# Kernel optimization log

Measured on AMD Instinct MI355X. Metric: run time of the kernel, lower is better.

## Reference

```python
import jax, jax.numpy as jnp
import numpy as np

DIM = 128
N_GNN = 3
B, N1, N2 = 8, 128, 512
VDW_N = 6.0
DEV_VDW = 0.2
MAX_VDW, MIN_VDW = 0.0356, 0.0178
DM_MIN = 0.5


def setup_inputs() -> dict:
    key = jax.random.key(0)
    ks = jax.random.split(key, 24)
    f32 = jnp.float32
    h1 = jax.random.normal(ks[0], (B, N1, 54), f32)
    h2 = jax.random.normal(ks[1], (B, N2, 54), f32)
    a1 = (jax.random.uniform(ks[2], (B, N1, N1)) < 0.1).astype(f32)
    adj1 = jnp.clip(a1 + jnp.swapaxes(a1, 1, 2) + jnp.eye(N1, dtype=f32), 0.0, 1.0)
    a2 = (jax.random.uniform(ks[3], (B, N2, N2)) < 0.05).astype(f32)
    adj2 = jnp.clip(a2 + jnp.swapaxes(a2, 1, 2) + jnp.eye(N2, dtype=f32), 0.0, 1.0)
    A_int = (jax.random.uniform(ks[4], (B, 8, N1, N2)) < 0.05).astype(f32)
    pos1 = jax.random.uniform(ks[5], (B, N1, 3), f32) * 30.0
    pos2 = jax.random.uniform(ks[6], (B, N2, 3), f32) * 30.0
    rotor = jax.random.uniform(ks[7], (B,), f32) * 10.0
    vdw_radius1 = 1.0 + jax.random.uniform(ks[8], (B, N1), f32)
    vdw_radius2 = 1.0 + jax.random.uniform(ks[9], (B, N2), f32)
    delta_uff = jax.random.uniform(ks[10], (B,), f32)
    no_metal1 = jnp.ones((B, N1), f32)
    no_metal2 = jnp.ones((B, N2), f32)
    s = 0.1
    node_W = jax.random.normal(ks[11], (54, DIM), f32) * s
    gat_W = jax.random.normal(ks[12], (N_GNN, DIM, DIM), f32) * s
    gat_b = jnp.zeros((N_GNN, DIM), f32)
    gat_A = jax.random.normal(ks[13], (N_GNN, DIM, DIM), f32) * s
    gate_W = jax.random.normal(ks[14], (N_GNN, 2 * DIM), f32) * s
    gate_b = jnp.zeros((N_GNN,), f32)
    vdwA_W1 = jax.random.normal(ks[15], (2 * DIM, 128), f32) * s
    vdwA_b1 = jnp.zeros((128,), f32)
    vdwA_W2 = jax.random.normal(ks[16], (128,), f32) * s
    vdwA_b2 = jnp.zeros((1,), f32)
    vdwB_W1 = jax.random.normal(ks[17], (2 * DIM, 128), f32) * s
    vdwB_b1 = jnp.zeros((128,), f32)
    vdwB_W2 = jax.random.normal(ks[18], (128,), f32) * s
    vdwB_b2 = jnp.zeros((1,), f32)
    hbond_coeff = jnp.array([1.0], f32)
    hydrophobic_coeff = jnp.array([0.5], f32)
    vdw_coeff = jnp.array([1.0], f32)
    rotor_coeff = jnp.array([0.5], f32)
    return dict(h1=h1, adj1=adj1, h2=h2, adj2=adj2, A_int=A_int, pos1=pos1, pos2=pos2,
                rotor=rotor, vdw_radius1=vdw_radius1, vdw_radius2=vdw_radius2,
                delta_uff=delta_uff, no_metal1=no_metal1, no_metal2=no_metal2,
                node_W=node_W, gat_W=gat_W, gat_b=gat_b, gat_A=gat_A, gate_W=gate_W,
                gate_b=gate_b, vdwA_W1=vdwA_W1, vdwA_b1=vdwA_b1, vdwA_W2=vdwA_W2,
                vdwA_b2=vdwA_b2, vdwB_W1=vdwB_W1, vdwB_b1=vdwB_b1, vdwB_W2=vdwB_W2,
                vdwB_b2=vdwB_b2, hbond_coeff=hbond_coeff,
                hydrophobic_coeff=hydrophobic_coeff, vdw_coeff=vdw_coeff,
                rotor_coeff=rotor_coeff)


def _gat(x, adj, W, b, A, gW, gb):
    # PIGNet GAT_gate: attention softmax over axis=1, masked by adj, gated residual.
    h = x @ W + b                                   # [B,N,D]
    e = jnp.einsum('bil,bkl->bik', h @ A, h)        # [B,N,N]
    e = e + jnp.swapaxes(e, 1, 2)
    att = jnp.where(adj > 0, e, -9e15)
    att = jax.nn.softmax(att, axis=1) * adj
    h_prime = jax.nn.relu(jnp.einsum('bij,bjk->bik', att, h))
    coeff = jax.nn.sigmoid(jnp.concatenate([x, h_prime], -1) @ gW + gb)[..., None]
    return coeff * x + (1.0 - coeff) * h_prime


def _pair_mlp(g1, g2, W1, b1, w2, b2):
    # Equivalent to Linear(cat[h1_rep,h2_rep]) without materializing the 2D concat.
    z = (jnp.einsum('bik,kh->bih', g1, W1[:DIM])[:, :, None, :]
         + jnp.einsum('bjk,kh->bjh', g2, W1[DIM:])[:, None, :, :] + b1)  # [B,N1,N2,128]
    return jax.nn.relu(z) @ w2 + b2                 # [B,N1,N2]


def _forward(h1, adj1, h2, adj2, A_int, pos1, pos2, rotor, vdw_radius1, vdw_radius2,
             delta_uff, no_metal1, no_metal2, node_W, gat_W, gat_b, gat_A, gate_W,
             gate_b, vdwA_W1, vdwA_b1, vdwA_W2, vdwA_b2, vdwB_W1, vdwB_b1, vdwB_W2,
             vdwB_b2, hbond_coeff, hydrophobic_coeff, vdw_coeff, rotor_coeff):
    g1 = h1 @ node_W
    g2 = h2 @ node_W
    for i in range(N_GNN):
        g1 = _gat(g1, adj1, gat_W[i], gat_b[i], gat_A[i], gate_W[i], gate_b[i])
        g2 = _gat(g2, adj2, gat_W[i], gat_b[i], gat_A[i], gate_W[i], gate_b[i])
    diff = pos1[:, :, None, :] - pos2[:, None, :, :]
    dm = jnp.sqrt(jnp.sum(diff * diff, -1) + 1e-10)   # [B,N1,N2]
    dm = jnp.where(dm < DM_MIN, 1e10, dm)
    A_w = jax.nn.sigmoid(_pair_mlp(g1, g2, vdwA_W1, vdwA_b1, vdwA_W2, vdwA_b2))
    B_w = jnp.tanh(_pair_mlp(g1, g2, vdwB_W1, vdwB_b1, vdwB_W2, vdwB_b2)) * DEV_VDW
    dm0 = vdw_radius1[:, :, None] + vdw_radius2[:, None, :] + B_w
    # vdW 12-6 term
    dm0_safe = jnp.where(dm0 < 1e-4, 1.0, dm0)
    rN = (dm0_safe / dm) ** VDW_N
    evdw = jnp.minimum(rN * rN - 2.0 * rN, 100.0)
    mask12 = no_metal1[:, :, None] * no_metal2[:, None, :]
    Aamp = A_w * (MAX_VDW - MIN_VDW) + MIN_VDW
    E_vdw = jnp.sum(Aamp * evdw * mask12, axis=(1, 2))
    # hbond / hydrophobic terms use unfixed dm0
    dmd = dm - dm0
    hb = -(hbond_coeff * hbond_coeff)[0]
    hy = -(hydrophobic_coeff * hydrophobic_coeff)[0]
    E_hb1 = jnp.sum(jnp.clip(dmd * A_int[:, 1] / -0.7, 0.0, 1.0), axis=(1, 2)) * hb
    E_hb2 = jnp.sum(jnp.clip(dmd * A_int[:, -1] / -0.7, 0.0, 1.0), axis=(1, 2)) * hb
    E_hp = jnp.sum(jnp.clip((-dmd + 1.5) * A_int[:, -2], 0.0, 1.0), axis=(1, 2)) * hy
    E_t = delta_uff * (vdw_coeff * vdw_coeff)[0]
    ret = jnp.stack([E_vdw, E_hb1, E_hb2, E_hp, E_t], -1)   # [B,5]
    ret = ret / (1.0 + (rotor_coeff * rotor_coeff)[0] * rotor[:, None])
    return ret


def reference(h1, adj1, h2, adj2, A_int, pos1, pos2, rotor, vdw_radius1, vdw_radius2,
              delta_uff, no_metal1, no_metal2, node_W, gat_W, gat_b, gat_A, gate_W,
              gate_b, vdwA_W1, vdwA_b1, vdwA_W2, vdwA_b2, vdwB_W1, vdwB_b1, vdwB_W2,
              vdwB_b2, hbond_coeff, hydrophobic_coeff, vdw_coeff, rotor_coeff):
    return _forward(h1, adj1, h2, adj2, A_int, pos1, pos2, rotor, vdw_radius1,
                    vdw_radius2, delta_uff, no_metal1, no_metal2, node_W, gat_W,
                    gat_b, gat_A, gate_W, gate_b, vdwA_W1, vdwA_b1, vdwA_W2,
                    vdwA_b2, vdwB_W1, vdwB_b1, vdwB_W2, vdwB_b2, hbond_coeff,
                    hydrophobic_coeff, vdw_coeff, rotor_coeff)
```

## Files before the change

### kernel.cpp

```cpp
#include <hip/hip_runtime.h>
#include <hip/hip_fp16.h>
#include <math.h>

#define D 128
#define NB 8
#define NN1 128
#define NN2 512
#define ROWS1 (NB * NN1)
#define ROWS2 (NB * NN2)
#define ROWS (ROWS1 + ROWS2)
#define CAP1 96
#define CAP2 160
#define CSR_ELEMS ((size_t)ROWS1 * CAP1 + (size_t)ROWS2 * CAP2)

typedef __half HT;

__device__ __forceinline__ void resolve_row(int row, int& base_row, size_t& cbase,
                                            int& N) {
    if (row < ROWS1) {
        base_row = row & ~127;
        cbase = (size_t)row * CAP1;
        N = NN1;
    } else {
        int r = row - ROWS1;
        base_row = ROWS1 + (r & ~511);
        cbase = (size_t)ROWS1 * CAP1 + (size_t)r * CAP2;
        N = NN2;
    }
}

__device__ __forceinline__ int swiz_row(int bid) {
    int batch = bid & 7, idx = bid >> 3;
    return (idx < NN1) ? batch * NN1 + idx
                       : ROWS1 + batch * NN2 + (idx - NN1);
}
__device__ __forceinline__ int swiz_row16(int bid) {
    int batch = bid & 7, gi = bid >> 3;
    return (gi < 8) ? batch * NN1 + gi * 16
                    : ROWS1 + batch * NN2 + (gi - 8) * 16;
}

__device__ __forceinline__ void load8h(const HT* p, float* o) {
    float4 raw = *(const float4*)p;
    const __half2* h2 = (const __half2*)&raw;
    float2 f0 = __half22float2(h2[0]);
    float2 f1 = __half22float2(h2[1]);
    float2 f2 = __half22float2(h2[2]);
    float2 f3 = __half22float2(h2[3]);
    o[0] = f0.x; o[1] = f0.y; o[2] = f1.x; o[3] = f1.y;
    o[4] = f2.x; o[5] = f2.y; o[6] = f3.x; o[7] = f3.y;
}

__global__ __launch_bounds__(128) void k_csrembed(
    const float* __restrict__ h1, const float* __restrict__ h2,
    const float* __restrict__ adj1, const float* __restrict__ adj2,
    const float* __restrict__ W, float* __restrict__ g,
    unsigned short* __restrict__ csr, int* __restrict__ nnz,
    float* __restrict__ out) {
    int row = swiz_row(blockIdx.x);
    int t = threadIdx.x;
    if (blockIdx.x == 0 && t < NB * 5) out[t] = 0.f;
    const float* src = (row < ROWS1) ? h1 + (size_t)row * 54
                                     : h2 + (size_t)(row - ROWS1) * 54;
    __shared__ float xr[56];
    if (t < 54) xr[t] = src[t];
    __syncthreads();
    float a0 = 0.f, a1 = 0.f;
#pragma unroll
    for (int k = 0; k < 54; k += 2) {
        a0 += xr[k] * W[k * D + t];
        if (k + 1 < 54) a1 += xr[k + 1] * W[(k + 1) * D + t];
    }
    g[(size_t)row * D + t] = a0 + a1;

    if (t < 64) {
        int base_row, N;
        size_t cbase;
        resolve_row(row, base_row, cbase, N);
        int cap = (row < ROWS1) ? CAP1 : CAP2;
        const float* arow = (row < ROWS1) ? adj1 + (size_t)row * NN1
                                          : adj2 + (size_t)(row - ROWS1) * NN2;
        int cnt = 0;
        for (int c0 = 0; c0 < N; c0 += 64) {
            float v = arow[c0 + t];
            unsigned long long m = __ballot(v > 0.f);
            int rank = __popcll(m & ((1ull << t) - 1ull));
            if (v > 0.f && cnt + rank < cap)
                csr[cbase + cnt + rank] = (unsigned short)(c0 + t);
            cnt += __popcll(m);
        }
        if (t == 0) nnz[row] = cnt < cap ? cnt : cap;
    }
}

__global__ __launch_bounds__(256) void k_h(const float* __restrict__ g,
                                           const float* __restrict__ W,
                                           const float* __restrict__ bias,
                                           const float* __restrict__ A,
                                           HT* __restrict__ h, HT* __restrict__ hA) {
    int row0 = swiz_row16(blockIdx.x);
    int t = threadIdx.x;
    int d = t & 127, rh = t >> 7;
    __shared__ float xs[16][D];
    __shared__ float hs[16][D];
    {
        int r = t >> 4, c = (t & 15) * 8;
        *(float4*)&xs[r][c] = *(const float4*)&g[((size_t)row0 + r) * D + c];
        *(float4*)&xs[r][c + 4] = *(const float4*)&g[((size_t)row0 + r) * D + c + 4];
    }
    __syncthreads();
    float bv = bias[d];
    float acc[8];
#pragma unroll
    for (int u = 0; u < 8; ++u) acc[u] = bv;
    for (int k0 = 0; k0 < D; k0 += 4) {
        float w0 = W[(k0 + 0) * D + d];
        float w1 = W[(k0 + 1) * D + d];
        float w2 = W[(k0 + 2) * D + d];
        float w3 = W[(k0 + 3) * D + d];
#pragma unroll
        for (int u = 0; u < 8; ++u) {
            float4 xv = *(const float4*)&xs[rh * 8 + u][k0];
            acc[u] += xv.x * w0 + xv.y * w1 + xv.z * w2 + xv.w * w3;
        }
    }
#pragma unroll
    for (int u = 0; u < 8; ++u) {
        int r = rh * 8 + u;
        h[((size_t)row0 + r) * D + d] = __float2half(acc[u]);
        hs[r][d] = acc[u];
    }
    __syncthreads();
    float acc2[8];
#pragma unroll
    for (int u = 0; u < 8; ++u) acc2[u] = 0.f;
    for (int k0 = 0; k0 < D; k0 += 4) {
        float w0 = A[(k0 + 0) * D + d];
        float w1 = A[(k0 + 1) * D + d];
        float w2 = A[(k0 + 2) * D + d];
        float w3 = A[(k0 + 3) * D + d];
#pragma unroll
        for (int u = 0; u < 8; ++u) {
            float4 xv = *(const float4*)&hs[rh * 8 + u][k0];
            acc2[u] += xv.x * w0 + xv.y * w1 + xv.z * w2 + xv.w * w3;
        }
    }
#pragma unroll
    for (int u = 0; u < 8; ++u)
        hA[((size_t)row0 + rh * 8 + u) * D + d] = __float2half(acc2[u]);
}

__global__ __launch_bounds__(128) void k_Ssp(const HT* __restrict__ h,
                                             const HT* __restrict__ hA,
                                             const unsigned short* __restrict__ csr,
                                             const int* __restrict__ nnz,
                                             float* __restrict__ svals,
                                             float2* __restrict__ rowstat) {
    int row = swiz_row(blockIdx.x);
    int t = threadIdx.x;
    int base_row, N;
    size_t cbase;
    resolve_row(row, base_row, cbase, N);
    int n = nnz[row];
    int grp = t >> 4, u = t & 15;
    float hi[8], ai[8];
    load8h(h + (size_t)row * D + u * 8, hi);
    load8h(hA + (size_t)row * D + u * 8, ai);
    __shared__ float sv[CAP2];
    for (int s0 = 0; s0 < n; s0 += 16) {
        int sa = s0 + grp;
        int sb = sa + 8;
        float pa = 0.f, pb = 0.f;
        if (sa < n) {
            int jrow = base_row + csr[cbase + sa];
            float hj[8], aj[8];
            load8h(h + (size_t)jrow * D + u * 8, hj);
            load8h(hA + (size_t)jrow * D + u * 8, aj);
#pragma unroll
            for (int q = 0; q < 8; ++q) pa += hi[q] * aj[q] + ai[q] * hj[q];
        }
        if (sb < n) {
            int jrow = base_row + csr[cbase + sb];
            float hj[8], aj[8];
            load8h(h + (size_t)jrow * D + u * 8, hj);
            load8h(hA + (size_t)jrow * D + u * 8, aj);
#pragma unroll
            for (int q = 0; q < 8; ++q) pb += hi[q] * aj[q] + ai[q] * hj[q];
        }
#pragma unroll
        for (int o = 8; o > 0; o >>= 1) {
            pa += __shfl_xor(pa, o);
            pb += __shfl_xor(pb, o);
        }
        if (u == 0) {
            if (sa < n) sv[sa] = pa;
            if (sb < n) sv[sb] = pb;
        }
    }
    __syncthreads();
    if (t < 64) {
        float m = -3.4e38f;
        for (int s = t; s < n; s += 64) m = fmaxf(m, sv[s]);
#pragma unroll
        for (int o = 32; o > 0; o >>= 1) m = fmaxf(m, __shfl_xor(m, o));
        float sum = 0.f;
        for (int s = t; s < n; s += 64) sum += expf(sv[s] - m);
#pragma unroll
        for (int o = 32; o > 0; o >>= 1) sum += __shfl_xor(sum, o);
        if (t == 0) rowstat[row] = make_float2(m, 1.f / sum);
    }
    for (int s = t; s < n; s += 128) svals[cbase + s] = sv[s];
}

__global__ __launch_bounds__(128) void k_hpgate(const HT* __restrict__ hbuf,
                                                float* __restrict__ g,
                                                const float* __restrict__ svals,
                                                const float2* __restrict__ rowstat,
                                                const unsigned short* __restrict__ csr,
                                                const int* __restrict__ nnz,
                                                const float* __restrict__ gW,
                                                const float* __restrict__ gb) {
    int row = swiz_row(blockIdx.x);
    int d = threadIdx.x;
    int base_row, N;
    size_t cbase;
    resolve_row(row, base_row, cbase, N);
    int n = nnz[row];
    __shared__ float avals[CAP2];
    __shared__ int aidx[CAP2];
    __shared__ float red[128];
    for (int s = d; s < n; s += 128) {
        int jrow = base_row + csr[cbase + s];
        float2 st = rowstat[jrow];
        avals[s] = expf(svals[cbase + s] - st.x) * st.y;
        aidx[s] = jrow;
    }
    __syncthreads();
    float a[8];
#pragma unroll
    for (int u = 0; u < 8; ++u) a[u] = 0.f;
    int s = 0;
    for (; s + 8 <= n; s += 8) {
#pragma unroll
        for (int u = 0; u < 8; ++u)
            a[u] += avals[s + u] * __half2float(hbuf[(size_t)aidx[s + u] * D + d]);
    }
    for (; s < n; ++s)
        a[0] += avals[s] * __half2float(hbuf[(size_t)aidx[s] * D + d]);
    float hv = fmaxf(((a[0] + a[1]) + (a[2] + a[3])) + ((a[4] + a[5]) + (a[6] + a[7])),
                     0.f);
    float xv = g[(size_t)row * D + d];
    red[d] = xv * gW[d] + hv * gW[D + d];
    __syncthreads();
    for (int o = 64; o > 0; o >>= 1) {
        if (d < o) red[d] += red[d + o];
        __syncthreads();
    }
    float c = 1.f / (1.f + expf(-(red[0] + gb[0])));
    g[(size_t)row * D + d] = c * xv + (1.f - c) * hv;
}

__global__ __launch_bounds__(256) void k_pairpre(const float* __restrict__ g,
                                                 const float* __restrict__ WA,
                                                 const float* __restrict__ WB,
                                                 const float* __restrict__ bA,
                                                 const float* __restrict__ bB,
                                                 float* __restrict__ aA,
                                                 float* __restrict__ aB) {
    int row0 = swiz_row16(blockIdx.x);
    int t = threadIdx.x;
    int d = t & 127, rh = t >> 7;
    int g2 = (row0 >= ROWS1);
    const float* WAp = g2 ? WA + D * D : WA;
    const float* WBp = g2 ? WB + D * D : WB;
    __shared__ float xs[16][D];
    {
        int r = t >> 4, c = (t & 15) * 8;
        *(float4*)&xs[r][c] = *(const float4*)&g[((size_t)row0 + r) * D + c];
        *(float4*)&xs[r][c + 4] = *(const float4*)&g[((size_t)row0 + r) * D + c + 4];
    }
    __syncthreads();
    float bvA = g2 ? 0.f : bA[d];
    float bvB = g2 ? 0.f : bB[d];
    float accA[8], accB[8];
#pragma unroll
    for (int u = 0; u < 8; ++u) { accA[u] = bvA; accB[u] = bvB; }
    for (int k0 = 0; k0 < D; k0 += 4) {
        float wa0 = WAp[(k0 + 0) * D + d], wa1 = WAp[(k0 + 1) * D + d];
        float wa2 = WAp[(k0 + 2) * D + d], wa3 = WAp[(k0 + 3) * D + d];
        float wb0 = WBp[(k0 + 0) * D + d], wb1 = WBp[(k0 + 1) * D + d];
        float wb2 = WBp[(k0 + 2) * D + d], wb3 = WBp[(k0 + 3) * D + d];
#pragma unroll
        for (int u = 0; u < 8; ++u) {
            float4 xv = *(const float4*)&xs[rh * 8 + u][k0];
            accA[u] += xv.x * wa0 + xv.y * wa1 + xv.z * wa2 + xv.w * wa3;
            accB[u] += xv.x * wb0 + xv.y * wb1 + xv.z * wb2 + xv.w * wb3;
        }
    }
#pragma unroll
    for (int u = 0; u < 8; ++u) {
        int r = rh * 8 + u;
        aA[((size_t)row0 + r) * D + d] = accA[u];
        aB[((size_t)row0 + r) * D + d] = accB[u];
    }
}

__global__ __launch_bounds__(256) void k_pairz(
    const float* __restrict__ aA, const float* __restrict__ aB,
    const float* __restrict__ w2A, const float* __restrict__ w2B,
    const float* __restrict__ b2A, const float* __restrict__ b2B,
    const float* __restrict__ pos1, const float* __restrict__ pos2,
    const float* __restrict__ vr1, const float* __restrict__ vr2,
    const float* __restrict__ nm1, const float* __restrict__ nm2,
    const float* __restrict__ A_int, const float* __restrict__ rotor,
    const float* __restrict__ duff, const float* __restrict__ hbond,
    const float* __restrict__ hydro, const float* __restrict__ vdwc,
    const float* __restrict__ rotc, float* __restrict__ out) {
    int b = blockIdx.x & 7;
    int tile = blockIdx.x >> 3;
    int itile = tile >> 4, jtile = tile & 15;
    int i0 = itile * 32, j0 = jtile * 32;
    int t = threadIdx.x;
    int tx = t & 15, ty = t >> 4;
    __shared__ float A1a[32][20], A1b[32][20], A2a[32][20], A2b[32][20];
    __shared__ float w2As[128], w2Bs[128];
    __shared__ float zAs[32][33], zBs[32][33];
    __shared__ float redc[8][4];
    if (t < 128) { w2As[t] = w2A[t]; w2Bs[t] = w2B[t]; }
    float zA[2][2] = {{0.f, 0.f}, {0.f, 0.f}};
    float zB[2][2] = {{0.f, 0.f}, {0.f, 0.f}};
    int half = t >> 7, idx = t & 127;
    int sr = idx >> 2, sc = (idx & 3) * 4;
    size_t grow = half ? (size_t)(ROWS1 + b * NN2 + j0 + sr)
                       : (size_t)(b * NN1 + i0 + sr);
    for (int hc = 0; hc < D; hc += 16) {
        __syncthreads();
        float4 va = *(const float4*)&aA[grow * D + hc + sc];
        float4 vb = *(const float4*)&aB[grow * D + hc + sc];
        if (half) { *(float4*)&A2a[sr][sc] = va; *(float4*)&A2b[sr][sc] = vb; }
        else      { *(float4*)&A1a[sr][sc] = va; *(float4*)&A1b[sr][sc] = vb; }
        __syncthreads();
#pragma unroll
        for (int hh = 0; hh < 16; hh += 4) {
            float4 wA = *(const float4*)&w2As[hc + hh];
            float4 wB = *(const float4*)&w2Bs[hc + hh];
            float4 xA0 = *(const float4*)&A1a[ty][hh];
            float4 xA1 = *(const float4*)&A1a[ty + 16][hh];
            float4 xB0 = *(const float4*)&A1b[ty][hh];
            float4 xB1 = *(const float4*)&A1b[ty + 16][hh];
            float4 yA0 = *(const float4*)&A2a[tx][hh];
            float4 yA1 = *(const float4*)&A2a[tx + 16][hh];
            float4 yB0 = *(const float4*)&A2b[tx][hh];
            float4 yB1 = *(const float4*)&A2b[tx + 16][hh];
#define RD4(xx, yy, ww) (fmaxf(xx.x + yy.x, 0.f) * ww.x + fmaxf(xx.y + yy.y, 0.f) * ww.y + \
                         fmaxf(xx.z + yy.z, 0.f) * ww.z + fmaxf(xx.w + yy.w, 0.f) * ww.w)
            zA[0][0] += RD4(xA0, yA0, wA); zA[0][1] += RD4(xA0, yA1, wA);
            zA[1][0] += RD4(xA1, yA0, wA); zA[1][1] += RD4(xA1, yA1, wA);
            zB[0][0] += RD4(xB0, yB0, wB); zB[0][1] += RD4(xB0, yB1, wB);
            zB[1][0] += RD4(xB1, yB0, wB); zB[1][1] += RD4(xB1, yB1, wB);
#undef RD4
        }
    }
#pragma unroll
    for (int u = 0; u < 2; ++u)
#pragma unroll
        for (int v = 0; v < 2; ++v) {
            zAs[ty + 16 * u][tx + 16 * v] = zA[u][v];
            zBs[ty + 16 * u][tx + 16 * v] = zB[u][v];
        }
    __syncthreads();
    int j2 = t & 31, ig = t >> 5;
    int jg = j0 + j2;
    size_t j_off = (size_t)b * NN2 + jg;
    float p2x = pos2[j_off * 3 + 0], p2y = pos2[j_off * 3 + 1], p2z = pos2[j_off * 3 + 2];
    float r2 = vr2[j_off], m2 = nm2[j_off];
    float zb2A = b2A[0], zb2B = b2B[0];
    float eV[4], e1[4], e2[4], eH[4];
#pragma unroll
    for (int ii = 0; ii < 4; ++ii) {
        int il = ig * 4 + ii;
        int iglob = i0 + il;
        size_t i_off = (size_t)b * NN1 + iglob;
        float zAv = zAs[il][j2] + zb2A;
        float zBv = zBs[il][j2] + zb2B;
        float dx = pos1[i_off * 3 + 0] - p2x;
        float dy = pos1[i_off * 3 + 1] - p2y;
        float dz = pos1[i_off * 3 + 2] - p2z;
        float dm = sqrtf(dx * dx + dy * dy + dz * dz + 1e-10f);
        if (dm < 0.5f) dm = 1e10f;
        float A_w = 1.f / (1.f + expf(-zAv));
        float B_w = tanhf(zBv) * 0.2f;
        float dm0 = vr1[i_off] + r2 + B_w;
        float dm0s = (dm0 < 1e-4f) ? 1.f : dm0;
        float rr = dm0s / dm;
        float rr2 = rr * rr;
        float rN = rr2 * rr2 * rr2;
        float evdw = fminf(rN * rN - 2.f * rN, 100.f);
        float mask = nm1[i_off] * m2;
        float Aamp = A_w * (0.0356f - 0.0178f) + 0.0178f;
        eV[ii] = Aamp * evdw * mask;
        float dmd = dm - dm0;
        size_t abase = (((size_t)b * 8) * NN1 + iglob) * NN2 + jg;
        float Ai1 = A_int[abase + (size_t)1 * NN1 * NN2];
        float Ai6 = A_int[abase + (size_t)6 * NN1 * NN2];
        float Ai7 = A_int[abase + (size_t)7 * NN1 * NN2];
        e1[ii] = fminf(fmaxf(dmd * Ai1 * (-1.f / 0.7f), 0.f), 1.f);
        e2[ii] = fminf(fmaxf(dmd * Ai7 * (-1.f / 0.7f), 0.f), 1.f);
        eH[ii] = fminf(fmaxf((1.5f - dmd) * Ai6, 0.f), 1.f);
    }
    float sV = (eV[0] + eV[1]) + (eV[2] + eV[3]);
    float s1 = (e1[0] + e1[1]) + (e1[2] + e1[3]);
    float s2 = (e2[0] + e2[1]) + (e2[2] + e2[3]);
    float sH = (eH[0] + eH[1]) + (eH[2] + eH[3]);
#pragma unroll
    for (int o = 16; o > 0; o >>= 1) {
        sV += __shfl_xor(sV, o);
        s1 += __shfl_xor(s1, o);
        s2 += __shfl_xor(s2, o);
        sH += __shfl_xor(sH, o);
    }
    if (j2 == 0) {
        redc[ig][0] = sV; redc[ig][1] = s1; redc[ig][2] = s2; redc[ig][3] = sH;
    }
    __syncthreads();
    if (t < 4) {
        float v = 0.f;
#pragma unroll
        for (int gg = 0; gg < 8; ++gg) v += redc[gg][t];
        float scl = 1.f / (1.f + rotc[0] * rotc[0] * rotor[b]);
        float coef;
        if (t == 0) coef = scl;
        else if (t == 3) coef = -hydro[0] * hydro[0] * scl;
        else coef = -hbond[0] * hbond[0] * scl;
        atomicAdd(&out[b * 5 + t], v * coef);
    }
    if (t == 4 && tile == 0) {
        float scl = 1.f / (1.f + rotc[0] * rotc[0] * rotor[b]);
        atomicAdd(&out[b * 5 + 4], duff[b] * vdwc[0] * vdwc[0] * scl);
    }
}

extern "C" void kernel_launch(void* const* d_in, const int* in_sizes, int n_in,
                              void* d_out, int out_size, void* d_ws, size_t ws_size,
                              hipStream_t stream) {
    const float* h1    = (const float*)d_in[0];
    const float* adj1  = (const float*)d_in[1];
    const float* h2    = (const float*)d_in[2];
    const float* adj2  = (const float*)d_in[3];
    const float* A_int = (const float*)d_in[4];
    const float* pos1  = (const float*)d_in[5];
    const float* pos2  = (const float*)d_in[6];
    const float* rotor = (const float*)d_in[7];
    const float* vr1   = (const float*)d_in[8];
    const float* vr2   = (const float*)d_in[9];
    const float* duff  = (const float*)d_in[10];
    const float* nm1   = (const float*)d_in[11];
    const float* nm2   = (const float*)d_in[12];
    const float* nodeW = (const float*)d_in[13];
    const float* gatW  = (const float*)d_in[14];
    const float* gatb  = (const float*)d_in[15];
    const float* gatA  = (const float*)d_in[16];
    const float* gateW = (const float*)d_in[17];
    const float* gateb = (const float*)d_in[18];
    const float* vA_W1 = (const float*)d_in[19];
    const float* vA_b1 = (const float*)d_in[20];
    const float* vA_W2 = (const float*)d_in[21];
    const float* vA_b2 = (const float*)d_in[22];
    const float* vB_W1 = (const float*)d_in[23];
    const float* vB_b1 = (const float*)d_in[24];
    const float* vB_W2 = (const float*)d_in[25];
    const float* vB_b2 = (const float*)d_in[26];
    const float* hbond = (const float*)d_in[27];
    const float* hydro = (const float*)d_in[28];
    const float* vdwc  = (const float*)d_in[29];
    const float* rotc  = (const float*)d_in[30];

    float* p = (float*)d_ws;
    float* g     = p; p += (size_t)ROWS * D;
    float* aA    = p; p += (size_t)ROWS * D;
    float* aB    = p; p += (size_t)ROWS * D;
    float* svals = p; p += CSR_ELEMS;
    float2* rowstat = (float2*)p; p += 2 * (size_t)ROWS;
    HT* hbuf  = (HT*)p; p += (size_t)ROWS * D / 2;
    HT* hAbuf = (HT*)p; p += (size_t)ROWS * D / 2;
    unsigned short* csr = (unsigned short*)p;
    int* nnz = (int*)(csr + CSR_ELEMS);
    float* outp = (float*)d_out;

    k_csrembed<<<ROWS, 128, 0, stream>>>(h1, h2, adj1, adj2, nodeW, g, csr, nnz, outp);

    for (int l = 0; l < 3; ++l) {
        const float* W  = gatW  + (size_t)l * D * D;
        const float* bb = gatb  + (size_t)l * D;
        const float* A  = gatA  + (size_t)l * D * D;
        const float* gW = gateW + (size_t)l * 2 * D;
        const float* gb = gateb + l;
        k_h<<<ROWS / 16, 256, 0, stream>>>(g, W, bb, A, hbuf, hAbuf);
        k_Ssp<<<ROWS, 128, 0, stream>>>(hbuf, hAbuf, csr, nnz, svals, rowstat);
        k_hpgate<<<ROWS, 128, 0, stream>>>(hbuf, g, svals, rowstat, csr, nnz, gW, gb);
    }

    k_pairpre<<<ROWS / 16, 256, 0, stream>>>(g, vA_W1, vB_W1, vA_b1, vB_b1, aA, aB);
    k_pairz<<<512, 256, 0, stream>>>(aA, aB, vA_W2, vB_W2, vA_b2, vB_b2,
                                     pos1, pos2, vr1, vr2, nm1, nm2, A_int,
                                     rotor, duff, hbond, hydro, vdwc, rotc, outp);
}
```

Baseline: 285.4 us.

## Fuse gate aggregation with next layer's GEMMs and embed into init kernel

Merges the per-row gated attention aggregation of one GNN layer with the next layer's h/hA GEMMs in a single kernel, and folds the node embedding and CSR build into the first layer's GEMM kernel. It double-buffers the h/hA half buffers so a kernel can read the old layer while writing the new one. Each block now handles 4 rows instead of 16 and uses wave-per-row gating with shuffle reductions. The aim is fewer launches and fewer round trips of g through global memory, at the cost of less weight reuse per block, since each weight load now serves 4 rows instead of 16.

```diff
diff --git a/kernel.cpp b/kernel.cpp
--- a/kernel.cpp
+++ b/kernel.cpp
@@ -29,15 +29,15 @@
     }
 }
 
+__device__ __forceinline__ int swiz_row4(int bid) {
+    int batch = bid & 7, gi = bid >> 3;
+    return (gi < 32) ? batch * NN1 + gi * 4
+                     : ROWS1 + batch * NN2 + (gi - 32) * 4;
+}
 __device__ __forceinline__ int swiz_row(int bid) {
     int batch = bid & 7, idx = bid >> 3;
     return (idx < NN1) ? batch * NN1 + idx
                        : ROWS1 + batch * NN2 + (idx - NN1);
-}
-__device__ __forceinline__ int swiz_row16(int bid) {
-    int batch = bid & 7, gi = bid >> 3;
-    return (gi < 8) ? batch * NN1 + gi * 16
-                    : ROWS1 + batch * NN2 + (gi - 8) * 16;
 }
 
 __device__ __forceinline__ void load8h(const HT* p, float* o) {
@@ -51,29 +51,72 @@
     o[4] = f2.x; o[5] = f2.y; o[6] = f3.x; o[7] = f3.y;
 }
 
-__global__ __launch_bounds__(128) void k_csrembed(
-    const float* __restrict__ h1, const float* __restrict__ h2,
+#define GEMM4(XS, W, BV, STMT0, STMT1)                                        \
+    {                                                                         \
+        float acc0 = (BV), acc1 = (BV);                                       \
+        for (int k0 = 0; k0 < D; k0 += 4) {                                   \
+            float w0 = (W)[(k0 + 0) * D + d];                                 \
+            float w1 = (W)[(k0 + 1) * D + d];                                 \
+            float w2 = (W)[(k0 + 2) * D + d];                                 \
+            float w3 = (W)[(k0 + 3) * D + d];                                 \
+            float4 x0 = *(const float4*)&XS[rh * 2 + 0][k0];                  \
+            float4 x1 = *(const float4*)&XS[rh * 2 + 1][k0];                  \
+            acc0 += x0.x * w0 + x0.y * w1 + x0.z * w2 + x0.w * w3;            \
+            acc1 += x1.x * w0 + x1.y * w1 + x1.z * w2 + x1.w * w3;            \
+        }                                                                     \
+        STMT0; STMT1;                                                         \
+    }
+
+__global__ __launch_bounds__(256) void k_init(
+    const float* __restrict__ h1in, const float* __restrict__ h2in,
     const float* __restrict__ adj1, const float* __restrict__ adj2,
-    const float* __restrict__ W, float* __restrict__ g,
+    const float* __restrict__ nodeW, const float* __restrict__ W,
+    const float* __restrict__ bias, const float* __restrict__ A,
+    float* __restrict__ g, HT* __restrict__ hOut, HT* __restrict__ hAOut,
     unsigned short* __restrict__ csr, int* __restrict__ nnz,
     float* __restrict__ out) {
-    int row = swiz_row(blockIdx.x);
+    int row0 = swiz_row4(blockIdx.x);
     int t = threadIdx.x;
     if (blockIdx.x == 0 && t < NB * 5) out[t] = 0.f;
-    const float* src = (row < ROWS1) ? h1 + (size_t)row * 54
-                                     : h2 + (size_t)(row - ROWS1) * 54;
-    __shared__ float xr[56];
-    if (t < 54) xr[t] = src[t];
-    __syncthreads();
-    float a0 = 0.f, a1 = 0.f;
-#pragma unroll
-    for (int k = 0; k < 54; k += 2) {
-        a0 += xr[k] * W[k * D + t];
-        if (k + 1 < 54) a1 += xr[k + 1] * W[(k + 1) * D + t];
-    }
-    g[(size_t)row * D + t] = a0 + a1;
-
-    if (t < 64) {
+    __shared__ float hin[4][54];
+    __shared__ float xs[4][D];
+    __shared__ float hs[4][D];
+    {
+        const float* src = (row0 < ROWS1) ? h1in + (size_t)row0 * 54
+                                          : h2in + (size_t)(row0 - ROWS1) * 54;
+        for (int idx = t; idx < 4 * 54; idx += 256) {
+            int r = idx / 54, c = idx - r * 54;
+            hin[r][c] = src[(size_t)r * 54 + c];
+        }
+    }
+    __syncthreads();
+    int d = t & 127, rh = t >> 7;
+    {
+        float e0 = 0.f, e1 = 0.f;
+        for (int k = 0; k < 54; ++k) {
+            float w = nodeW[k * D + d];
+            e0 += hin[rh * 2 + 0][k] * w;
+            e1 += hin[rh * 2 + 1][k] * w;
+        }
+        xs[rh * 2 + 0][d] = e0;
+        xs[rh * 2 + 1][d] = e1;
+        g[((size_t)row0 + rh * 2 + 0) * D + d] = e0;
+        g[((size_t)row0 + rh * 2 + 1) * D + d] = e1;
+    }
+    __syncthreads();
+    float bv = bias[d];
+    GEMM4(xs, W, bv,
+          { hs[rh * 2 + 0][d] = acc0;
+            hOut[((size_t)row0 + rh * 2 + 0) * D + d] = __float2half(acc0); },
+          { hs[rh * 2 + 1][d] = acc1;
+            hOut[((size_t)row0 + rh * 2 + 1) * D + d] = __float2half(acc1); })
+    __syncthreads();
+    GEMM4(hs, A, 0.f,
+          { hAOut[((size_t)row0 + rh * 2 + 0) * D + d] = __float2half(acc0); },
+          { hAOut[((size_t)row0 + rh * 2 + 1) * D + d] = __float2half(acc1); })
+    {
+        int lane = t & 63, wv = t >> 6;
+        int row = row0 + wv;
         int base_row, N;
         size_t cbase;
         resolve_row(row, base_row, cbase, N);
@@ -82,72 +125,15 @@
                                           : adj2 + (size_t)(row - ROWS1) * NN2;
         int cnt = 0;
         for (int c0 = 0; c0 < N; c0 += 64) {
-            float v = arow[c0 + t];
+            float v = arow[c0 + lane];
             unsigned long long m = __ballot(v > 0.f);
-            int rank = __popcll(m & ((1ull << t) - 1ull));
+            int rank = __popcll(m & ((1ull << lane) - 1ull));
             if (v > 0.f && cnt + rank < cap)
-                csr[cbase + cnt + rank] = (unsigned short)(c0 + t);
+                csr[cbase + cnt + rank] = (unsigned short)(c0 + lane);
             cnt += __popcll(m);
         }
-        if (t == 0) nnz[row] = cnt < cap ? cnt : cap;
-    }
-}
-
-__global__ __launch_bounds__(256) void k_h(const float* __restrict__ g,
-                                           const float* __restrict__ W,
-                                           const float* __restrict__ bias,
-                                           const float* __restrict__ A,
-                                           HT* __restrict__ h, HT* __restrict__ hA) {
-    int row0 = swiz_row16(blockIdx.x);
-    int t = threadIdx.x;
-    int d = t & 127, rh = t >> 7;
-    __shared__ float xs[16][D];
-    __shared__ float hs[16][D];
-    {
-        int r = t >> 4, c = (t & 15) * 8;
-        *(float4*)&xs[r][c] = *(const float4*)&g[((size_t)row0 + r) * D + c];
-        *(float4*)&xs[r][c + 4] = *(const float4*)&g[((size_t)row0 + r) * D + c + 4];
-    }
-    __syncthreads();
-    float bv = bias[d];
-    float acc[8];
-#pragma unroll
-    for (int u = 0; u < 8; ++u) acc[u] = bv;
-    for (int k0 = 0; k0 < D; k0 += 4) {
-        float w0 = W[(k0 + 0) * D + d];
-        float w1 = W[(k0 + 1) * D + d];
-        float w2 = W[(k0 + 2) * D + d];
-        float w3 = W[(k0 + 3) * D + d];
-#pragma unroll
-        for (int u = 0; u < 8; ++u) {
-            float4 xv = *(const float4*)&xs[rh * 8 + u][k0];
-            acc[u] += xv.x * w0 + xv.y * w1 + xv.z * w2 + xv.w * w3;
-        }
-    }
-#pragma unroll
-    for (int u = 0; u < 8; ++u) {
-        int r = rh * 8 + u;
-        h[((size_t)row0 + r) * D + d] = __float2half(acc[u]);
-        hs[r][d] = acc[u];
-    }
-    __syncthreads();
-    float acc2[8];
-#pragma unroll
-    for (int u = 0; u < 8; ++u) acc2[u] = 0.f;
-    for (int k0 = 0; k0 < D; k0 += 4) {
-        float w0 = A[(k0 + 0) * D + d];
-        float w1 = A[(k0 + 1) * D + d];
-        float w2 = A[(k0 + 2) * D + d];
-        float w3 = A[(k0 + 3) * D + d];
-#pragma unroll
-        for (int u = 0; u < 8; ++u) {
-            float4 xv = *(const float4*)&hs[rh * 8 + u][k0];
-            acc2[u] += xv.x * w0 + xv.y * w1 + xv.z * w2 + xv.w * w3;
-        }
-    }
-#pragma unroll
-    for (int u = 0; u < 8; ++u)
-        hA[((size_t)row0 + rh * 8 + u) * D + d] = __float2half(acc2[u]);
+        if (lane == 0) nnz[row] = cnt < cap ? cnt : cap;
+    }
 }
 
 __global__ __launch_bounds__(128) void k_Ssp(const HT* __restrict__ h,
@@ -212,97 +198,118 @@
     for (int s = t; s < n; s += 128) svals[cbase + s] = sv[s];
 }
 
-__global__ __launch_bounds__(128) void k_hpgate(const HT* __restrict__ hbuf,
-                                                float* __restrict__ g,
-                                                const float* __restrict__ svals,
-                                                const float2* __restrict__ rowstat,
-                                                const unsigned short* __restrict__ csr,
-                                                const int* __restrict__ nnz,
-                                                const float* __restrict__ gW,
-                                                const float* __restrict__ gb) {
-    int row = swiz_row(blockIdx.x);
-    int d = threadIdx.x;
+__device__ __forceinline__ void gate4(
+    int row0, int t, const HT* __restrict__ hIn, float* __restrict__ g,
+    const float* __restrict__ svals, const float2* __restrict__ rowstat,
+    const unsigned short* __restrict__ csr, const int* __restrict__ nnz,
+    const float* __restrict__ gW, float gb0, float (*xs)[D],
+    float av[4][CAP2], unsigned short ax[4][CAP2]) {
+    int lane = t & 63, wv = t >> 6;
+    int row = row0 + wv;
     int base_row, N;
     size_t cbase;
     resolve_row(row, base_row, cbase, N);
     int n = nnz[row];
-    __shared__ float avals[CAP2];
-    __shared__ int aidx[CAP2];
-    __shared__ float red[128];
-    for (int s = d; s < n; s += 128) {
-        int jrow = base_row + csr[cbase + s];
-        float2 st = rowstat[jrow];
-        avals[s] = expf(svals[cbase + s] - st.x) * st.y;
-        aidx[s] = jrow;
-    }
-    __syncthreads();
-    float a[8];
-#pragma unroll
-    for (int u = 0; u < 8; ++u) a[u] = 0.f;
+    for (int s = lane; s < n; s += 64) {
+        int jl = csr[cbase + s];
+        float2 st = rowstat[base_row + jl];
+        av[wv][s] = expf(svals[cbase + s] - st.x) * st.y;
+        ax[wv][s] = (unsigned short)jl;
+    }
+    const __half2* hb2 = (const __half2*)hIn;
+    size_t boff = ((size_t)base_row << 6) + lane;
+    float2 a[8];
+#pragma unroll
+    for (int u = 0; u < 8; ++u) a[u] = make_float2(0.f, 0.f);
     int s = 0;
     for (; s + 8 <= n; s += 8) {
 #pragma unroll
-        for (int u = 0; u < 8; ++u)
-            a[u] += avals[s + u] * __half2float(hbuf[(size_t)aidx[s + u] * D + d]);
-    }
-    for (; s < n; ++s)
-        a[0] += avals[s] * __half2float(hbuf[(size_t)aidx[s] * D + d]);
-    float hv = fmaxf(((a[0] + a[1]) + (a[2] + a[3])) + ((a[4] + a[5]) + (a[6] + a[7])),
-                     0.f);
-    float xv = g[(size_t)row * D + d];
-    red[d] = xv * gW[d] + hv * gW[D + d];
-    __syncthreads();
-    for (int o = 64; o > 0; o >>= 1) {
-        if (d < o) red[d] += red[d + o];
-        __syncthreads();
-    }
-    float c = 1.f / (1.f + expf(-(red[0] + gb[0])));
-    g[(size_t)row * D + d] = c * xv + (1.f - c) * hv;
-}
-
-__global__ __launch_bounds__(256) void k_pairpre(const float* __restrict__ g,
-                                                 const float* __restrict__ WA,
-                                                 const float* __restrict__ WB,
-                                                 const float* __restrict__ bA,
-                                                 const float* __restrict__ bB,
-                                                 float* __restrict__ aA,
-                                                 float* __restrict__ aB) {
-    int row0 = swiz_row16(blockIdx.x);
+        for (int u = 0; u < 8; ++u) {
+            float avv = av[wv][s + u];
+            float2 f = __half22float2(hb2[boff + ((size_t)ax[wv][s + u] << 6)]);
+            a[u].x += avv * f.x;
+            a[u].y += avv * f.y;
+        }
+    }
+    for (; s < n; ++s) {
+        float avv = av[wv][s];
+        float2 f = __half22float2(hb2[boff + ((size_t)ax[wv][s] << 6)]);
+        a[0].x += avv * f.x;
+        a[0].y += avv * f.y;
+    }
+    float hv0 = fmaxf(((a[0].x + a[1].x) + (a[2].x + a[3].x)) +
+                      ((a[4].x + a[5].x) + (a[6].x + a[7].x)), 0.f);
+    float hv1 = fmaxf(((a[0].y + a[1].y) + (a[2].y + a[3].y)) +
+                      ((a[4].y + a[5].y) + (a[6].y + a[7].y)), 0.f);
+    float2 xv = *(const float2*)&g[(size_t)row * D + 2 * lane];
+    float2 w01 = *(const float2*)&gW[2 * lane];
+    float2 w23 = *(const float2*)&gW[D + 2 * lane];
+    float part = xv.x * w01.x + xv.y * w01.y + hv0 * w23.x + hv1 * w23.y;
+#pragma unroll
+    for (int o = 32; o > 0; o >>= 1) part += __shfl_xor(part, o);
+    float c = 1.f / (1.f + expf(-(part + gb0)));
+    float g0 = c * xv.x + (1.f - c) * hv0;
+    float g1 = c * xv.y + (1.f - c) * hv1;
+    xs[wv][2 * lane] = g0;
+    xs[wv][2 * lane + 1] = g1;
+    *(float2*)&g[(size_t)row * D + 2 * lane] = make_float2(g0, g1);
+}
+
+__global__ __launch_bounds__(256) void k_gh(
+    const HT* __restrict__ hIn, float* __restrict__ g,
+    const float* __restrict__ svals, const float2* __restrict__ rowstat,
+    const unsigned short* __restrict__ csr, const int* __restrict__ nnz,
+    const float* __restrict__ gW, const float* __restrict__ gb,
+    const float* __restrict__ W, const float* __restrict__ bias,
+    const float* __restrict__ A, HT* __restrict__ hOut, HT* __restrict__ hAOut) {
+    int row0 = swiz_row4(blockIdx.x);
     int t = threadIdx.x;
+    __shared__ float xs[4][D];
+    __shared__ float hs[4][D];
+    __shared__ float av[4][CAP2];
+    __shared__ unsigned short ax[4][CAP2];
+    gate4(row0, t, hIn, g, svals, rowstat, csr, nnz, gW, gb[0], xs, av, ax);
+    __syncthreads();
+    int d = t & 127, rh = t >> 7;
+    float bv = bias[d];
+    GEMM4(xs, W, bv,
+          { hs[rh * 2 + 0][d] = acc0;
+            hOut[((size_t)row0 + rh * 2 + 0) * D + d] = __float2half(acc0); },
+          { hs[rh * 2 + 1][d] = acc1;
+            hOut[((size_t)row0 + rh * 2 + 1) * D + d] = __float2half(acc1); })
+    __syncthreads();
+    GEMM4(hs, A, 0.f,
+          { hAOut[((size_t)row0 + rh * 2 + 0) * D + d] = __float2half(acc0); },
+          { hAOut[((size_t)row0 + rh * 2 + 1) * D + d] = __float2half(acc1); })
+}
+
+__global__ __launch_bounds__(256) void k_gp(
+    const HT* __restrict__ hIn, float* __restrict__ g,
+    const float* __restrict__ svals, const float2* __restrict__ rowstat,
+    const unsigned short* __restrict__ csr, const int* __restrict__ nnz,
+    const float* __restrict__ gW, const float* __restrict__ gb,
+    const float* __restrict__ WA, const float* __restrict__ WB,
+    const float* __restrict__ bA, const float* __restrict__ bB,
+    float* __restrict__ aA, float* __restrict__ aB) {
+    int row0 = swiz_row4(blockIdx.x);
+    int t = threadIdx.x;
+    __shared__ float xs[4][D];
+    __shared__ float av[4][CAP2];
+    __shared__ unsigned short ax[4][CAP2];
+    gate4(row0, t, hIn, g, svals, rowstat, csr, nnz, gW, gb[0], xs, av, ax);
+    __syncthreads();
     int d = t & 127, rh = t >> 7;
     int g2 = (row0 >= ROWS1);
     const float* WAp = g2 ? WA + D * D : WA;
     const float* WBp = g2 ? WB + D * D : WB;
-    __shared__ float xs[16][D];
-    {
-        int r = t >> 4, c = (t & 15) * 8;
-        *(float4*)&xs[r][c] = *(const float4*)&g[((size_t)row0 + r) * D + c];
-        *(float4*)&xs[r][c + 4] = *(const float4*)&g[((size_t)row0 + r) * D + c + 4];
-    }
-    __syncthreads();
     float bvA = g2 ? 0.f : bA[d];
     float bvB = g2 ? 0.f : bB[d];
-    float accA[8], accB[8];
-#pragma unroll
-    for (int u = 0; u < 8; ++u) { accA[u] = bvA; accB[u] = bvB; }
-    for (int k0 = 0; k0 < D; k0 += 4) {
-        float wa0 = WAp[(k0 + 0) * D + d], wa1 = WAp[(k0 + 1) * D + d];
-        float wa2 = WAp[(k0 + 2) * D + d], wa3 = WAp[(k0 + 3) * D + d];
-        float wb0 = WBp[(k0 + 0) * D + d], wb1 = WBp[(k0 + 1) * D + d];
-        float wb2 = WBp[(k0 + 2) * D + d], wb3 = WBp[(k0 + 3) * D + d];
-#pragma unroll
-        for (int u = 0; u < 8; ++u) {
-            float4 xv = *(const float4*)&xs[rh * 8 + u][k0];
-            accA[u] += xv.x * wa0 + xv.y * wa1 + xv.z * wa2 + xv.w * wa3;
-            accB[u] += xv.x * wb0 + xv.y * wb1 + xv.z * wb2 + xv.w * wb3;
-        }
-    }
-#pragma unroll
-    for (int u = 0; u < 8; ++u) {
-        int r = rh * 8 + u;
-        aA[((size_t)row0 + r) * D + d] = accA[u];
-        aB[((size_t)row0 + r) * D + d] = accB[u];
-    }
+    GEMM4(xs, WAp, bvA,
+          { aA[((size_t)row0 + rh * 2 + 0) * D + d] = acc0; },
+          { aA[((size_t)row0 + rh * 2 + 1) * D + d] = acc1; })
+    GEMM4(xs, WBp, bvB,
+          { aB[((size_t)row0 + rh * 2 + 0) * D + d] = acc0; },
+          { aB[((size_t)row0 + rh * 2 + 1) * D + d] = acc1; })
 }
 
 __global__ __launch_bounds__(256) void k_pairz(
@@ -481,26 +488,31 @@
     float* aB    = p; p += (size_t)ROWS * D;
     float* svals = p; p += CSR_ELEMS;
     float2* rowstat = (float2*)p; p += 2 * (size_t)ROWS;
-    HT* hbuf  = (HT*)p; p += (size_t)ROWS * D / 2;
-    HT* hAbuf = (HT*)p; p += (size_t)ROWS * D / 2;
+    HT* hb0 = (HT*)p; p += (size_t)ROWS * D / 2;
+    HT* hA0 = (HT*)p; p += (size_t)ROWS * D / 2;
+    HT* hb1 = (HT*)p; p += (size_t)ROWS * D / 2;
+    HT* hA1 = (HT*)p; p += (size_t)ROWS * D / 2;
     unsigned short* csr = (unsigned short*)p;
     int* nnz = (int*)(csr + CSR_ELEMS);
     float* outp = (float*)d_out;
 
-    k_csrembed<<<ROWS, 128, 0, stream>>>(h1, h2, adj1, adj2, nodeW, g, csr, nnz, outp);
-
-    for (int l = 0; l < 3; ++l) {
-        const float* W  = gatW  + (size_t)l * D * D;
-        const float* bb = gatb  + (size_t)l * D;
-        const float* A  = gatA  + (size_t)l * D * D;
-        const float* gW = gateW + (size_t)l * 2 * D;
-        const float* gb = gateb + l;
-        k_h<<<ROWS / 16, 256, 0, stream>>>(g, W, bb, A, hbuf, hAbuf);
-        k_Ssp<<<ROWS, 128, 0, stream>>>(hbuf, hAbuf, csr, nnz, svals, rowstat);
-        k_hpgate<<<ROWS, 128, 0, stream>>>(hbuf, g, svals, rowstat, csr, nnz, gW, gb);
-    }
-
-    k_pairpre<<<ROWS / 16, 256, 0, stream>>>(g, vA_W1, vB_W1, vA_b1, vB_b1, aA, aB);
+    k_init<<<ROWS / 4, 256, 0, stream>>>(h1, h2, adj1, adj2, nodeW, gatW, gatb, gatA,
+                                         g, hb0, hA0, csr, nnz, outp);
+    k_Ssp<<<ROWS, 128, 0, stream>>>(hb0, hA0, csr, nnz, svals, rowstat);
+    k_gh<<<ROWS / 4, 256, 0, stream>>>(hb0, g, svals, rowstat, csr, nnz,
+                                       gateW, gateb,
+                                       gatW + (size_t)1 * D * D, gatb + D,
+                                       gatA + (size_t)1 * D * D, hb1, hA1);
+    k_Ssp<<<ROWS, 128, 0, stream>>>(hb1, hA1, csr, nnz, svals, rowstat);
+    k_gh<<<ROWS / 4, 256, 0, stream>>>(hb1, g, svals, rowstat, csr, nnz,
+                                       gateW + 2 * D, gateb + 1,
+                                       gatW + (size_t)2 * D * D, gatb + 2 * D,
+                                       gatA + (size_t)2 * D * D, hb0, hA0);
+    k_Ssp<<<ROWS, 128, 0, stream>>>(hb0, hA0, csr, nnz, svals, rowstat);
+    k_gp<<<ROWS / 4, 256, 0, stream>>>(hb0, g, svals, rowstat, csr, nnz,
+                                       gateW + 4 * D, gateb + 2,
+                                       vA_W1, vB_W1, vA_b1, vB_b1, aA, aB);
+
     k_pairz<<<512, 256, 0, stream>>>(aA, aB, vA_W2, vB_W2, vA_b2, vB_b2,
                                      pos1, pos2, vr1, vr2, nm1, nm2, A_int,
                                      rotor, duff, hbond, hydro, vdwc, rotc, outp);
```

Result: faster. 261.5 us (-8.4%).
